# Optimization experiments

Measured on AMD Instinct MI355X. Metric: run time of the kernel, lower is better.

Reference implementation:

```python
import jax, jax.numpy as jnp
import numpy as np

HM = 256  # output_hm_shape


def _peak_grid(heatmap):
    # max_num_peaks=1 NMS -> global argmax per (b, joint) channel
    B, J, H, W = heatmap.shape
    idx = jnp.argmax(heatmap.reshape(B, J, H * W), axis=-1)
    y = (idx // W).astype(jnp.float32)
    x = (idx % W).astype(jnp.float32)
    ny = (H - 1) / 2.0
    nx = (W - 1) / 2.0
    # normalized (gx, gy) in [-1, 1], note (row,col) -> (x,y) flip as in source
    return jnp.stack([(x - nx) / nx, (y - ny) / ny], axis=-1)  # [B, J, 2]


def _bilinear_sample(feat, grid):
    # feat: [B, C, H, W], grid: [B, N, 2] (gx, gy), align_corners=True
    B, C, H, W = feat.shape
    x = (grid[..., 0] + 1.0) * 0.5 * (W - 1)
    y = (grid[..., 1] + 1.0) * 0.5 * (H - 1)
    x0 = jnp.floor(x); y0 = jnp.floor(y)
    wx = x - x0; wy = y - y0
    x0i = jnp.clip(x0, 0, W - 1).astype(jnp.int32)
    x1i = jnp.clip(x0 + 1, 0, W - 1).astype(jnp.int32)
    y0i = jnp.clip(y0, 0, H - 1).astype(jnp.int32)
    y1i = jnp.clip(y0 + 1, 0, H - 1).astype(jnp.int32)
    ff = feat.reshape(B, C, H * W)
    def g(iy, ix):
        return jnp.take_along_axis(ff, (iy * W + ix)[:, None, :], axis=2)  # [B, C, N]
    wx = wx[:, None, :]; wy = wy[:, None, :]
    return (g(y0i, x0i) * (1 - wx) * (1 - wy) + g(y0i, x1i) * wx * (1 - wy)
            + g(y1i, x0i) * (1 - wx) * wy + g(y1i, x1i) * wx * wy)


def _nearest_sample(feat, grid):
    B, C, H, W = feat.shape
    ix = jnp.clip(jnp.round((grid[..., 0] + 1.0) * 0.5 * (W - 1)), 0, W - 1).astype(jnp.int32)
    iy = jnp.clip(jnp.round((grid[..., 1] + 1.0) * 0.5 * (H - 1)), 0, H - 1).astype(jnp.int32)
    ff = feat.reshape(B, C, H * W)
    return jnp.take_along_axis(ff, (iy * W + ix)[:, None, :], axis=2)  # [B, C, N]


def _mlp(x, Ws, bs):
    # ReLU on every layer including last (is_activation_last=True)
    for W, b in zip(Ws, bs):
        x = jax.nn.relu(x @ W + b)
    return x


def setup_inputs() -> dict:
    key = jax.random.key(0)
    ks = jax.random.split(key, 16)
    inp = {
        'heatmap': jax.random.normal(ks[0], (16, 64, HM, HM), jnp.float32),
        'pos_embed': jax.random.normal(ks[1], (16, 32, HM, HM), jnp.float32),
        'feat1': jax.random.normal(ks[2], (16, 96, 128, 128), jnp.float32),
        'feat2': jax.random.normal(ks[3], (16, 384, 64, 64), jnp.float32),
        'feat3': jax.random.normal(ks[4], (16, 512, 32, 32), jnp.float32),
    }
    dims = [992, 1024, 512, 256, 224]
    for i in range(4):
        fan = dims[i]
        inp[f'W{i+1}'] = jax.random.normal(ks[5 + i], (dims[i], dims[i + 1]), jnp.float32) / np.sqrt(fan)
        inp[f'b{i+1}'] = jnp.zeros((dims[i + 1],), jnp.float32)
    return inp


def reference(heatmap, pos_embed, feat1, feat2, feat3, W1, b1, W2, b2, W3, b3, W4, b4):
    grid = _peak_grid(heatmap)  # [B, J, 2], detached in original (cpu numpy)
    positions = _nearest_sample(pos_embed, grid)  # [B, 32, J]
    ms = jnp.concatenate([_bilinear_sample(feat1, grid),
                          _bilinear_sample(feat2, grid),
                          _bilinear_sample(feat3, grid)], axis=1)  # [B, 992, J]
    seq = _mlp(ms.transpose(0, 2, 1), [W1, W2, W3, W4], [b1, b2, b3, b4])  # [B, J, 224]
    input_seq = jnp.concatenate([seq.transpose(0, 2, 1), positions], axis=1)  # [B, 256, J]
    return input_seq
```

## Files before the change

### kernel.cpp

```cpp
#include <hip/hip_runtime.h>
#include <hip/hip_bf16.h>
#include <cstddef>
#include <cstdint>


typedef __attribute__((ext_vector_type(8))) short bf16x8;
typedef __attribute__((ext_vector_type(4))) float f32x4;

__device__ inline void bilinear_block(const float* __restrict__ fb, int C, int H, int W,
                                      float gx, float gy,
                                      __hip_bfloat16* __restrict__ dst, int tid) {
    const float x = (gx + 1.0f) * 0.5f * (float)(W - 1);
    const float y = (gy + 1.0f) * 0.5f * (float)(H - 1);
    const float x0f = floorf(x), y0f = floorf(y);
    const float wx = x - x0f, wy = y - y0f;
    const int x0 = (int)fminf(fmaxf(x0f,       0.f), (float)(W - 1));
    const int x1 = (int)fminf(fmaxf(x0f + 1.f, 0.f), (float)(W - 1));
    const int y0 = (int)fminf(fmaxf(y0f,       0.f), (float)(H - 1));
    const int y1 = (int)fminf(fmaxf(y0f + 1.f, 0.f), (float)(H - 1));
    const float w00 = (1.f - wx) * (1.f - wy);
    const float w01 = wx * (1.f - wy);
    const float w10 = (1.f - wx) * wy;
    const float w11 = wx * wy;
    const int i00 = y0 * W + x0, i01 = y0 * W + x1;
    const int i10 = y1 * W + x0, i11 = y1 * W + x1;
    const size_t HW = (size_t)H * W;
    for (int c = tid; c < C; c += 256) {
        const float* fc = fb + (size_t)c * HW;
        float v = fc[i00] * w00 + fc[i01] * w01 + fc[i10] * w10 + fc[i11] * w11;
        dst[c] = __float2bfloat16(v);
    }
}

__global__ __launch_bounds__(256) void fused_front_kernel(
    const float* __restrict__ hm,
    const float* __restrict__ pos_embed,
    const float* __restrict__ feat1, const float* __restrict__ feat2,
    const float* __restrict__ feat3,
    const float* __restrict__ W1, const float* __restrict__ W2,
    const float* __restrict__ W3, const float* __restrict__ W4,
    __hip_bfloat16* __restrict__ T1, __hip_bfloat16* __restrict__ T2,
    __hip_bfloat16* __restrict__ T3, __hip_bfloat16* __restrict__ T4,
    __hip_bfloat16* __restrict__ X0, float* __restrict__ out) {
    __shared__ float smem[32 * 33];
    float* sval = smem;
    int*   sidx = (int*)(smem + 256);
    const int tid = threadIdx.x;

    if (blockIdx.x >= 1024) {
        int bid = blockIdx.x - 1024;
        const float* W; __hip_bfloat16* T; int K, N;
        if (bid < 992)        { W = W1; T = T1; K = 992;  N = 1024; }
        else if (bid < 1504)  { bid -= 992;  W = W2; T = T2; K = 1024; N = 512; }
        else if (bid < 1632)  { bid -= 1504; W = W3; T = T3; K = 512;  N = 256; }
        else                  { bid -= 1632; W = W4; T = T4; K = 256;  N = 224; }
        const int tilesN = N >> 5;
        const int tk = bid / tilesN, tn = bid - tk * tilesN;
        float (*tile)[33] = (float(*)[33])smem;
        const int col = tid & 31, rowg = tid >> 5;
        #pragma unroll
        for (int i = 0; i < 4; ++i) {
            int k = (tk << 5) + rowg + (i << 3);
            tile[rowg + (i << 3)][col] = W[(size_t)k * N + (tn << 5) + col];
        }
        __syncthreads();
        #pragma unroll
        for (int i = 0; i < 4; ++i) {
            int n = (tn << 5) + rowg + (i << 3);
            T[(size_t)n * K + (tk << 5) + col] = __float2bfloat16(tile[col][rowg + (i << 3)]);
        }
        return;
    }

    const int plane = blockIdx.x;
    const float4* p4 = (const float4*)(hm + (size_t)plane * 65536);
    float best = -3.402823466e38f;
    int bidx = 0;
    for (int i = tid; i < 16384; i += 256) {
        float4 v = p4[i];
        int base = i << 2;
        if (v.x > best) { best = v.x; bidx = base; }
        if (v.y > best) { best = v.y; bidx = base + 1; }
        if (v.z > best) { best = v.z; bidx = base + 2; }
        if (v.w > best) { best = v.w; bidx = base + 3; }
    }
    sval[tid] = best; sidx[tid] = bidx;
    __syncthreads();
    for (int s = 128; s > 0; s >>= 1) {
        if (tid < s) {
            float ov = sval[tid + s]; int oi = sidx[tid + s];
            if (ov > sval[tid] || (ov == sval[tid] && oi < sidx[tid])) {
                sval[tid] = ov; sidx[tid] = oi;
            }
        }
        __syncthreads();
    }
    const int idx = sidx[0];

    const int b = plane >> 6, j = plane & 63;
    const int py = idx >> 8, px = idx & 255;
    const float gx = ((float)px - 127.5f) / 127.5f;
    const float gy = ((float)py - 127.5f) / 127.5f;

    if (tid < 32) {
        float v = pos_embed[((size_t)(b * 32 + tid)) * 65536 + idx];
        out[(size_t)b * 16384 + (size_t)(224 + tid) * 64 + j] = v;
    }

    __hip_bfloat16* xrow = X0 + (size_t)plane * 992;
    bilinear_block(feat1 + (size_t)b *  96 * 128 * 128,  96, 128, 128, gx, gy, xrow,       tid);
    bilinear_block(feat2 + (size_t)b * 384 *  64 *  64, 384,  64,  64, gx, gy, xrow +  96, tid);
    bilinear_block(feat3 + (size_t)b * 512 *  32 *  32, 512,  32,  32, gx, gy, xrow + 480, tid);
}

template<bool LAST>
__global__ __launch_bounds__(64) void mfma_gemm(
    const short* __restrict__ A, const short* __restrict__ Bt,
    const float* __restrict__ bias, void* __restrict__ Yv,
    int N, int K) {
    const int lane = threadIdx.x;
    const int q = lane >> 4, r = lane & 15;
    const int m0 = blockIdx.y << 5;
    const int n0 = blockIdx.x << 5;

    const short* pa0 = A  + (size_t)(m0 + r) * K + (q << 3);
    const short* pa1 = pa0 + (size_t)16 * K;
    const short* pb0 = Bt + (size_t)(n0 + r) * K + (q << 3);
    const short* pb1 = pb0 + (size_t)16 * K;

    f32x4 acc00 = {0.f,0.f,0.f,0.f}, acc01 = {0.f,0.f,0.f,0.f};
    f32x4 acc10 = {0.f,0.f,0.f,0.f}, acc11 = {0.f,0.f,0.f,0.f};

    bf16x8 a0 = *(const bf16x8*)pa0;
    bf16x8 a1 = *(const bf16x8*)pa1;
    bf16x8 b0 = *(const bf16x8*)pb0;
    bf16x8 b1 = *(const bf16x8*)pb1;

    for (int k = 32; k < K; k += 32) {
        bf16x8 na0 = *(const bf16x8*)(pa0 + k);
        bf16x8 na1 = *(const bf16x8*)(pa1 + k);
        bf16x8 nb0 = *(const bf16x8*)(pb0 + k);
        bf16x8 nb1 = *(const bf16x8*)(pb1 + k);
        acc00 = __builtin_amdgcn_mfma_f32_16x16x32_bf16(a0, b0, acc00, 0, 0, 0);
        acc01 = __builtin_amdgcn_mfma_f32_16x16x32_bf16(a0, b1, acc01, 0, 0, 0);
        acc10 = __builtin_amdgcn_mfma_f32_16x16x32_bf16(a1, b0, acc10, 0, 0, 0);
        acc11 = __builtin_amdgcn_mfma_f32_16x16x32_bf16(a1, b1, acc11, 0, 0, 0);
        a0 = na0; a1 = na1; b0 = nb0; b1 = nb1;
    }
    acc00 = __builtin_amdgcn_mfma_f32_16x16x32_bf16(a0, b0, acc00, 0, 0, 0);
    acc01 = __builtin_amdgcn_mfma_f32_16x16x32_bf16(a0, b1, acc01, 0, 0, 0);
    acc10 = __builtin_amdgcn_mfma_f32_16x16x32_bf16(a1, b0, acc10, 0, 0, 0);
    acc11 = __builtin_amdgcn_mfma_f32_16x16x32_bf16(a1, b1, acc11, 0, 0, 0);

    const float bias0 = bias[n0 + r];
    const float bias1 = bias[n0 + 16 + r];
    #pragma unroll
    for (int i = 0; i < 4; ++i) {
        const int row0 = m0 + (q << 2) + i;
        const int row1 = row0 + 16;
        float v00 = fmaxf(acc00[i] + bias0, 0.f);
        float v01 = fmaxf(acc01[i] + bias1, 0.f);
        float v10 = fmaxf(acc10[i] + bias0, 0.f);
        float v11 = fmaxf(acc11[i] + bias1, 0.f);
        if (LAST) {
            float* O = (float*)Yv;
            const int b0r = row0 >> 6, j0 = row0 & 63;
            const int b1r = row1 >> 6, j1 = row1 & 63;
            O[(size_t)b0r * 16384 + (size_t)(n0 + r)      * 64 + j0] = v00;
            O[(size_t)b0r * 16384 + (size_t)(n0 + 16 + r) * 64 + j0] = v01;
            O[(size_t)b1r * 16384 + (size_t)(n0 + r)      * 64 + j1] = v10;
            O[(size_t)b1r * 16384 + (size_t)(n0 + 16 + r) * 64 + j1] = v11;
        } else {
            __hip_bfloat16* Y = (__hip_bfloat16*)Yv;
            Y[(size_t)row0 * N + n0 + r]      = __float2bfloat16(v00);
            Y[(size_t)row0 * N + n0 + 16 + r] = __float2bfloat16(v01);
            Y[(size_t)row1 * N + n0 + r]      = __float2bfloat16(v10);
            Y[(size_t)row1 * N + n0 + 16 + r] = __float2bfloat16(v11);
        }
    }
}

extern "C" void kernel_launch(void* const* d_in, const int* in_sizes, int n_in,
                              void* d_out, int out_size, void* d_ws, size_t ws_size,
                              hipStream_t stream) {
    (void)in_sizes; (void)n_in; (void)out_size; (void)ws_size;
    const float* heatmap   = (const float*)d_in[0];
    const float* pos_embed = (const float*)d_in[1];
    const float* feat1     = (const float*)d_in[2];
    const float* feat2     = (const float*)d_in[3];
    const float* feat3     = (const float*)d_in[4];
    const float* W1 = (const float*)d_in[5];  const float* b1 = (const float*)d_in[6];
    const float* W2 = (const float*)d_in[7];  const float* b2 = (const float*)d_in[8];
    const float* W3 = (const float*)d_in[9];  const float* b3 = (const float*)d_in[10];
    const float* W4 = (const float*)d_in[11]; const float* b4 = (const float*)d_in[12];
    float* out = (float*)d_out;

    char* ws = (char*)d_ws;
    short* X0 = (short*)(ws + 8192);
    short* X1 = X0 + (size_t)1024 * 992;
    short* X2 = X1 + (size_t)1024 * 1024;
    short* X3 = X2 + (size_t)1024 * 512;
    short* T1 = X3 + (size_t)1024 * 256;
    short* T2 = T1 + (size_t)1024 * 992;
    short* T3 = T2 + (size_t)512 * 1024;
    short* T4 = T3 + (size_t)256 * 512;

    fused_front_kernel<<<2712, 256, 0, stream>>>(
        heatmap, pos_embed, feat1, feat2, feat3,
        W1, W2, W3, W4,
        (__hip_bfloat16*)T1, (__hip_bfloat16*)T2, (__hip_bfloat16*)T3, (__hip_bfloat16*)T4,
        (__hip_bfloat16*)X0, out);
    mfma_gemm<false><<<dim3(32, 32), 64, 0, stream>>>(X0, T1, b1, X1, 1024,  992);
    mfma_gemm<false><<<dim3(16, 32), 64, 0, stream>>>(X1, T2, b2, X2,  512, 1024);
    mfma_gemm<false><<<dim3( 8, 32), 64, 0, stream>>>(X2, T3, b3, X3,  256,  512);
    mfma_gemm<true ><<<dim3( 7, 32), 64, 0, stream>>>(X3, T4, b4, out, 224,  256);
}
```

Baseline: 594.4 us.

## Split GEMM K-loop across four waves and use wave-shuffle argmax reduction

Each GEMM block now runs four waves that each handle an interleaved quarter of the K steps. Partial accumulators are summed through shared memory before bias and ReLU, which shortens the serial MFMA dependency chain per output tile. The argmax block reduction in the front kernel uses wavefront shuffles plus a four-entry shared-memory merge instead of a multi-barrier tree. The cost is extra shared-memory traffic and a barrier in the GEMM epilogue.

```diff
diff --git a/kernel.cpp b/kernel.cpp
--- a/kernel.cpp
+++ b/kernel.cpp
@@ -44,7 +44,7 @@
     __hip_bfloat16* __restrict__ X0, float* __restrict__ out) {
     __shared__ float smem[32 * 33];
     float* sval = smem;
-    int*   sidx = (int*)(smem + 256);
+    int*   sidx = (int*)(smem + 4);
     const int tid = threadIdx.x;
 
     if (blockIdx.x >= 1024) {
@@ -84,18 +84,21 @@
         if (v.z > best) { best = v.z; bidx = base + 2; }
         if (v.w > best) { best = v.w; bidx = base + 3; }
     }
-    sval[tid] = best; sidx[tid] = bidx;
+    #pragma unroll
+    for (int off = 32; off > 0; off >>= 1) {
+        float ov = __shfl_down(best, off);
+        int   oi = __shfl_down(bidx, off);
+        if (ov > best || (ov == best && oi < bidx)) { best = ov; bidx = oi; }
+    }
+    if ((tid & 63) == 0) { sval[tid >> 6] = best; sidx[tid >> 6] = bidx; }
     __syncthreads();
-    for (int s = 128; s > 0; s >>= 1) {
-        if (tid < s) {
-            float ov = sval[tid + s]; int oi = sidx[tid + s];
-            if (ov > sval[tid] || (ov == sval[tid] && oi < sidx[tid])) {
-                sval[tid] = ov; sidx[tid] = oi;
-            }
-        }
-        __syncthreads();
-    }
-    const int idx = sidx[0];
+    float bv = sval[0]; int bi = sidx[0];
+    #pragma unroll
+    for (int w2 = 1; w2 < 4; ++w2) {
+        float ov = sval[w2]; int oi = sidx[w2];
+        if (ov > bv || (ov == bv && oi < bi)) { bv = ov; bi = oi; }
+    }
+    const int idx = bi;
 
     const int b = plane >> 6, j = plane & 63;
     const int py = idx >> 8, px = idx & 255;
@@ -114,11 +117,13 @@
 }
 
 template<bool LAST>
-__global__ __launch_bounds__(64) void mfma_gemm(
+__global__ __launch_bounds__(256) void mfma_gemm_sk(
     const short* __restrict__ A, const short* __restrict__ Bt,
     const float* __restrict__ bias, void* __restrict__ Yv,
     int N, int K) {
-    const int lane = threadIdx.x;
+    __shared__ float red[4 * 64 * 17];
+    const int tid = threadIdx.x;
+    const int w = tid >> 6, lane = tid & 63;
     const int q = lane >> 4, r = lane & 15;
     const int m0 = blockIdx.y << 5;
     const int n0 = blockIdx.x << 5;
@@ -131,51 +136,59 @@
     f32x4 acc00 = {0.f,0.f,0.f,0.f}, acc01 = {0.f,0.f,0.f,0.f};
     f32x4 acc10 = {0.f,0.f,0.f,0.f}, acc11 = {0.f,0.f,0.f,0.f};
 
-    bf16x8 a0 = *(const bf16x8*)pa0;
-    bf16x8 a1 = *(const bf16x8*)pa1;
-    bf16x8 b0 = *(const bf16x8*)pb0;
-    bf16x8 b1 = *(const bf16x8*)pb1;
-
-    for (int k = 32; k < K; k += 32) {
-        bf16x8 na0 = *(const bf16x8*)(pa0 + k);
-        bf16x8 na1 = *(const bf16x8*)(pa1 + k);
-        bf16x8 nb0 = *(const bf16x8*)(pb0 + k);
-        bf16x8 nb1 = *(const bf16x8*)(pb1 + k);
+    const int nk = K >> 5;
+    int ks = w;
+    {
+        int off = ks << 5;
+        bf16x8 a0 = *(const bf16x8*)(pa0 + off);
+        bf16x8 a1 = *(const bf16x8*)(pa1 + off);
+        bf16x8 b0 = *(const bf16x8*)(pb0 + off);
+        bf16x8 b1 = *(const bf16x8*)(pb1 + off);
+        for (ks += 4; ks < nk; ks += 4) {
+            int o2 = ks << 5;
+            bf16x8 na0 = *(const bf16x8*)(pa0 + o2);
+            bf16x8 na1 = *(const bf16x8*)(pa1 + o2);
+            bf16x8 nb0 = *(const bf16x8*)(pb0 + o2);
+            bf16x8 nb1 = *(const bf16x8*)(pb1 + o2);
+            acc00 = __builtin_amdgcn_mfma_f32_16x16x32_bf16(a0, b0, acc00, 0, 0, 0);
+            acc01 = __builtin_amdgcn_mfma_f32_16x16x32_bf16(a0, b1, acc01, 0, 0, 0);
+            acc10 = __builtin_amdgcn_mfma_f32_16x16x32_bf16(a1, b0, acc10, 0, 0, 0);
+            acc11 = __builtin_amdgcn_mfma_f32_16x16x32_bf16(a1, b1, acc11, 0, 0, 0);
+            a0 = na0; a1 = na1; b0 = nb0; b1 = nb1;
+        }
         acc00 = __builtin_amdgcn_mfma_f32_16x16x32_bf16(a0, b0, acc00, 0, 0, 0);
         acc01 = __builtin_amdgcn_mfma_f32_16x16x32_bf16(a0, b1, acc01, 0, 0, 0);
         acc10 = __builtin_amdgcn_mfma_f32_16x16x32_bf16(a1, b0, acc10, 0, 0, 0);
         acc11 = __builtin_amdgcn_mfma_f32_16x16x32_bf16(a1, b1, acc11, 0, 0, 0);
-        a0 = na0; a1 = na1; b0 = nb0; b1 = nb1;
-    }
-    acc00 = __builtin_amdgcn_mfma_f32_16x16x32_bf16(a0, b0, acc00, 0, 0, 0);
-    acc01 = __builtin_amdgcn_mfma_f32_16x16x32_bf16(a0, b1, acc01, 0, 0, 0);
-    acc10 = __builtin_amdgcn_mfma_f32_16x16x32_bf16(a1, b0, acc10, 0, 0, 0);
-    acc11 = __builtin_amdgcn_mfma_f32_16x16x32_bf16(a1, b1, acc11, 0, 0, 0);
-
-    const float bias0 = bias[n0 + r];
-    const float bias1 = bias[n0 + 16 + r];
+    }
+
+    float* myrow = red + (size_t)(w * 64 + lane) * 17;
     #pragma unroll
     for (int i = 0; i < 4; ++i) {
-        const int row0 = m0 + (q << 2) + i;
-        const int row1 = row0 + 16;
-        float v00 = fmaxf(acc00[i] + bias0, 0.f);
-        float v01 = fmaxf(acc01[i] + bias1, 0.f);
-        float v10 = fmaxf(acc10[i] + bias0, 0.f);
-        float v11 = fmaxf(acc11[i] + bias1, 0.f);
+        myrow[i]      = acc00[i];
+        myrow[4 + i]  = acc01[i];
+        myrow[8 + i]  = acc10[i];
+        myrow[12 + i] = acc11[i];
+    }
+    __syncthreads();
+
+    #pragma unroll
+    for (int jj = 0; jj < 4; ++jj) {
+        const int e = tid + (jj << 8);
+        const int le = e >> 4, s = e & 15;
+        const int which = s >> 2, i = s & 3;
+        float v = red[(0 * 64 + le) * 17 + s] + red[(1 * 64 + le) * 17 + s]
+                + red[(2 * 64 + le) * 17 + s] + red[(3 * 64 + le) * 17 + s];
+        const int qe = le >> 4, re = le & 15;
+        const int row = m0 + (qe << 2) + i + ((which & 2) ? 16 : 0);
+        const int col = n0 + re + ((which & 1) ? 16 : 0);
+        v = fmaxf(v + bias[col], 0.f);
         if (LAST) {
             float* O = (float*)Yv;
-            const int b0r = row0 >> 6, j0 = row0 & 63;
-            const int b1r = row1 >> 6, j1 = row1 & 63;
-            O[(size_t)b0r * 16384 + (size_t)(n0 + r)      * 64 + j0] = v00;
-            O[(size_t)b0r * 16384 + (size_t)(n0 + 16 + r) * 64 + j0] = v01;
-            O[(size_t)b1r * 16384 + (size_t)(n0 + r)      * 64 + j1] = v10;
-            O[(size_t)b1r * 16384 + (size_t)(n0 + 16 + r) * 64 + j1] = v11;
+            O[(size_t)(row >> 6) * 16384 + (size_t)col * 64 + (row & 63)] = v;
         } else {
             __hip_bfloat16* Y = (__hip_bfloat16*)Yv;
-            Y[(size_t)row0 * N + n0 + r]      = __float2bfloat16(v00);
-            Y[(size_t)row0 * N + n0 + 16 + r] = __float2bfloat16(v01);
-            Y[(size_t)row1 * N + n0 + r]      = __float2bfloat16(v10);
-            Y[(size_t)row1 * N + n0 + 16 + r] = __float2bfloat16(v11);
+            Y[(size_t)row * N + col] = __float2bfloat16(v);
         }
     }
 }
@@ -210,8 +223,8 @@
         W1, W2, W3, W4,
         (__hip_bfloat16*)T1, (__hip_bfloat16*)T2, (__hip_bfloat16*)T3, (__hip_bfloat16*)T4,
         (__hip_bfloat16*)X0, out);
-    mfma_gemm<false><<<dim3(32, 32), 64, 0, stream>>>(X0, T1, b1, X1, 1024,  992);
-    mfma_gemm<false><<<dim3(16, 32), 64, 0, stream>>>(X1, T2, b2, X2,  512, 1024);
-    mfma_gemm<false><<<dim3( 8, 32), 64, 0, stream>>>(X2, T3, b3, X3,  256,  512);
-    mfma_gemm<true ><<<dim3( 7, 32), 64, 0, stream>>>(X3, T4, b4, out, 224,  256);
-}
+    mfma_gemm_sk<false><<<dim3(32, 32), 256, 0, stream>>>(X0, T1, b1, X1, 1024,  992);
+    mfma_gemm_sk<false><<<dim3(16, 32), 256, 0, stream>>>(X1, T2, b2, X2,  512, 1024);
+    mfma_gemm_sk<false><<<dim3( 8, 32), 256, 0, stream>>>(X2, T3, b3, X3,  256,  512);
+    mfma_gemm_sk<true ><<<dim3( 7, 32), 256, 0, stream>>>(X3, T4, b4, out,  224,  256);
+}
```

Result: faster. 578.1 us (-2.7%).
